# Kernel optimization log

Measured on AMD Instinct MI355X. Metric: run time of the kernel, lower is better.

## Reference

```python
import jax, jax.numpy as jnp
import numpy as np

D_MODEL = 1024
N_HEADS = 16
K_RETRIEVED = 32
BANK_SIZE = 131072
EPS = 1e-12  # matches F.normalize eps


def setup_inputs() -> dict:
    key = jax.random.key(0)
    ks = jax.random.split(key, 7)
    B, T = 8, 2048
    x = jax.random.normal(ks[0], (B, T, D_MODEL), dtype=jnp.float32)
    mem_keys = jax.random.normal(ks[1], (BANK_SIZE, D_MODEL), dtype=jnp.float32)
    mem_values = jax.random.normal(ks[2], (BANK_SIZE, D_MODEL), dtype=jnp.float32)
    s = 1.0 / np.sqrt(D_MODEL)
    Wq = jax.random.normal(ks[3], (D_MODEL, D_MODEL), dtype=jnp.float32) * s
    Wk = jax.random.normal(ks[4], (D_MODEL, D_MODEL), dtype=jnp.float32) * s
    Wv = jax.random.normal(ks[5], (D_MODEL, D_MODEL), dtype=jnp.float32) * s
    Wo = jax.random.normal(ks[6], (D_MODEL, D_MODEL), dtype=jnp.float32) * s
    gate_logit = jnp.zeros((1,), dtype=jnp.float32)
    return {"x": x, "mem_keys": mem_keys, "mem_values": mem_values,
            "Wq": Wq, "Wk": Wk, "Wv": Wv, "Wo": Wo, "gate_logit": gate_logit}


def _normalize(v):
    n = jnp.linalg.norm(v, axis=-1, keepdims=True)
    return v / jnp.maximum(n, EPS)


def reference(x, mem_keys, mem_values, Wq, Wk, Wv, Wo, gate_logit):
    B, T, D = x.shape
    H, hd, k = N_HEADS, D_MODEL // N_HEADS, K_RETRIEVED

    # --- retrieval: mean-pool query, cosine-sim top-k, gather values ---
    q = x.mean(axis=1)                       # (B, D)
    sims = _normalize(q) @ _normalize(mem_keys).T   # (B, BANK_SIZE)
    _, idx = jax.lax.top_k(sims, k)          # (B, k) descending
    retrieved = mem_values[idx]              # (B, k, d_mem)

    # --- cross-attention over retrieved docs ---
    Q = (x @ Wq).reshape(B, T, H, hd)
    K = (retrieved @ Wk).reshape(B, k, H, hd)
    V = (retrieved @ Wv).reshape(B, k, H, hd)
    scale = 1.0 / jnp.sqrt(jnp.asarray(hd, dtype=x.dtype))
    attn = jnp.einsum('bthd,bkhd->bhtk', Q, K) * scale
    attn = jax.nn.softmax(attn, axis=-1)
    ctx = jnp.einsum('bhtk,bkhd->bthd', attn, V).reshape(B, T, D)
    ctx = ctx @ Wo

    gate = jax.nn.sigmoid(gate_logit)        # (1,) broadcasts
    return x + gate * ctx
```

## Files before the change

### kernel.cpp

```cpp
#include <hip/hip_runtime.h>

#define D_MODEL 1024
#define NH 16
#define HD 64
#define KRET 32
#define BANK 131072
#define BB 8
#define TT 2048
#define MTOK 16384
#define EPSN 1e-12f

typedef __attribute__((ext_vector_type(8))) short bf16x8;
typedef __attribute__((ext_vector_type(8))) unsigned short u16x8;
typedef __attribute__((ext_vector_type(4))) float f32x4;

__device__ __forceinline__ unsigned short f2bf(float f) {
  unsigned int u = __float_as_uint(f);
  u += 0x7fffu + ((u >> 16) & 1u);
  return (unsigned short)(u >> 16);
}
__device__ __forceinline__ float bf2f(unsigned short h) {
  return __uint_as_float(((unsigned int)h) << 16);
}

__device__ __forceinline__ void gload16(const void* g, void* l) {
  __builtin_amdgcn_global_load_lds(
      (const __attribute__((address_space(1))) unsigned int*)g,
      (__attribute__((address_space(3))) unsigned int*)l, 16, 0, 0);
}

__global__ __launch_bounds__(256) void k_conv_mean(const float* __restrict__ x,
                                                   unsigned short* __restrict__ xb,
                                                   float* __restrict__ part) {
  int ch = blockIdx.x, b = blockIdx.y, tid = threadIdx.x;
  const float4* xp = (const float4*)(x + ((size_t)b * TT + ch * 32) * D_MODEL);
  ushort4* xo = (ushort4*)(xb + ((size_t)b * TT + ch * 32) * D_MODEL);
  float4 acc = {0.f, 0.f, 0.f, 0.f};
#pragma unroll 4
  for (int t = 0; t < 32; t++) {
    float4 v = xp[t * 256 + tid];
    acc.x += v.x; acc.y += v.y; acc.z += v.z; acc.w += v.w;
    ushort4 o;
    o.x = f2bf(v.x); o.y = f2bf(v.y); o.z = f2bf(v.z); o.w = f2bf(v.w);
    xo[t * 256 + tid] = o;
  }
  ((float4*)part)[((size_t)b * 64 + ch) * 256 + tid] = acc;
}

__global__ __launch_bounds__(256) void k_transW(const float* W0, const float* W1,
                                                const float* W2, const float* W3,
                                                unsigned short* T0, unsigned short* T1,
                                                unsigned short* T2, unsigned short* T3) {
  const float* W; unsigned short* T;
  switch (blockIdx.z) {
    case 0: W = W0; T = T0; break;
    case 1: W = W1; T = T1; break;
    case 2: W = W2; T = T2; break;
    default: W = W3; T = T3; break;
  }
  __shared__ float tile[64][65];
  int k0 = blockIdx.y * 64, n0 = blockIdx.x * 64;
  int tid = threadIdx.x;
#pragma unroll
  for (int i = 0; i < 16; i++) {
    int idx = tid + i * 256; int r = idx >> 6, c = idx & 63;
    tile[r][c] = W[(size_t)(k0 + r) * D_MODEL + n0 + c];
  }
  __syncthreads();
#pragma unroll
  for (int i = 0; i < 16; i++) {
    int idx = tid + i * 256; int r = idx >> 6, c = idx & 63;
    T[(size_t)(n0 + r) * D_MODEL + k0 + c] = f2bf(tile[c][r]);
  }
}

__global__ __launch_bounds__(256) void k_qnorm(const float* __restrict__ part,
                                               float* __restrict__ qn) {
  int b = blockIdx.x; int tid = threadIdx.x;
  __shared__ float red[4];
  const float4* pp = (const float4*)part + (size_t)b * 64 * 256 + tid;
  float4 a = {0.f, 0.f, 0.f, 0.f};
#pragma unroll 8
  for (int p = 0; p < 64; p++) {
    float4 v = pp[(size_t)p * 256];
    a.x += v.x; a.y += v.y; a.z += v.z; a.w += v.w;
  }
  const float sc = 1.f / (float)TT;
  a.x *= sc; a.y *= sc; a.z *= sc; a.w *= sc;
  float ss = a.x * a.x + a.y * a.y + a.z * a.z + a.w * a.w;
#pragma unroll
  for (int m = 32; m >= 1; m >>= 1) ss += __shfl_xor(ss, m);
  if ((tid & 63) == 0) red[tid >> 6] = ss;
  __syncthreads();
  float tot = red[0] + red[1] + red[2] + red[3];
  float inv = 1.f / fmaxf(sqrtf(tot), EPSN);
  float4 o = {a.x * inv, a.y * inv, a.z * inv, a.w * inv};
  ((float4*)qn)[(size_t)b * 256 + tid] = o;
}

__global__ __launch_bounds__(256) void k_sims(const float* __restrict__ mk,
                                              const float* __restrict__ qn,
                                              float* __restrict__ sims) {
  int wave = threadIdx.x >> 6, lane = threadIdx.x & 63;
  int row0 = (blockIdx.x * 4 + wave) * 4;
  float4 kv[4][4];
#pragma unroll
  for (int r = 0; r < 4; r++) {
    const float4* kr = (const float4*)(mk + (size_t)(row0 + r) * D_MODEL);
#pragma unroll
    for (int i = 0; i < 4; i++) kv[r][i] = kr[lane + 64 * i];
  }
  float ss[4] = {0.f, 0.f, 0.f, 0.f};
#pragma unroll
  for (int r = 0; r < 4; r++)
#pragma unroll
    for (int i = 0; i < 4; i++)
      ss[r] += kv[r][i].x * kv[r][i].x + kv[r][i].y * kv[r][i].y +
               kv[r][i].z * kv[r][i].z + kv[r][i].w * kv[r][i].w;
  float dots[8][4];
#pragma unroll
  for (int b = 0; b < 8; b++)
#pragma unroll
    for (int r = 0; r < 4; r++) dots[b][r] = 0.f;
#pragma unroll
  for (int b = 0; b < 8; b++) {
    const float4* qb = (const float4*)(qn + (size_t)b * D_MODEL);
#pragma unroll
    for (int i = 0; i < 4; i++) {
      float4 q4 = qb[lane + 64 * i];
#pragma unroll
      for (int r = 0; r < 4; r++)
        dots[b][r] += kv[r][i].x * q4.x + kv[r][i].y * q4.y +
                      kv[r][i].z * q4.z + kv[r][i].w * q4.w;
    }
  }
#pragma unroll
  for (int m = 32; m >= 1; m >>= 1) {
#pragma unroll
    for (int r = 0; r < 4; r++) ss[r] += __shfl_xor(ss[r], m);
#pragma unroll
    for (int b = 0; b < 8; b++)
#pragma unroll
      for (int r = 0; r < 4; r++) dots[b][r] += __shfl_xor(dots[b][r], m);
  }
  if (lane == 0) {
#pragma unroll
    for (int r = 0; r < 4; r++) {
      float inv = 1.f / fmaxf(sqrtf(ss[r]), EPSN);
#pragma unroll
      for (int b = 0; b < 8; b++)
        sims[(size_t)b * BANK + row0 + r] = dots[b][r] * inv;
    }
  }
}

__global__ __launch_bounds__(256) void k_topk_local(const float* __restrict__ sims,
                                                    float* __restrict__ cval,
                                                    int* __restrict__ cidx) {
  int b = blockIdx.y, chunk = blockIdx.x;
  int tid = threadIdx.x, wave = tid >> 6, lane = tid & 63;
  const float* sb = sims + (size_t)b * BANK + chunk * 2048;
  float v[8]; int gi[8];
#pragma unroll
  for (int j = 0; j < 8; j++) {
    int loc = j * 256 + tid;
    v[j] = sb[loc];
    gi[j] = chunk * 2048 + loc;
  }
  __shared__ float wv[4]; __shared__ int wi[4];
  __shared__ int bcast;
  for (int it = 0; it < KRET; ++it) {
    float best = -1e30f; int besti = 1 << 30;
#pragma unroll
    for (int j = 0; j < 8; j++)
      if (v[j] > best || (v[j] == best && gi[j] < besti)) { best = v[j]; besti = gi[j]; }
#pragma unroll
    for (int m = 32; m >= 1; m >>= 1) {
      float ov = __shfl_xor(best, m); int oi = __shfl_xor(besti, m);
      if (ov > best || (ov == best && oi < besti)) { best = ov; besti = oi; }
    }
    if (lane == 0) { wv[wave] = best; wi[wave] = besti; }
    __syncthreads();
    if (tid == 0) {
      float fb = wv[0]; int fi = wi[0];
      for (int w = 1; w < 4; w++)
        if (wv[w] > fb || (wv[w] == fb && wi[w] < fi)) { fb = wv[w]; fi = wi[w]; }
      bcast = fi;
      cval[((size_t)b * 64 + chunk) * KRET + it] = fb;
      cidx[((size_t)b * 64 + chunk) * KRET + it] = fi;
    }
    __syncthreads();
    int w = bcast;
#pragma unroll
    for (int j = 0; j < 8; j++)
      if (gi[j] == w) v[j] = -1e30f;
  }
}

__global__ __launch_bounds__(256) void k_topk_merge(const float* __restrict__ cval,
                                                    const int* __restrict__ cidx,
                                                    int* __restrict__ idx) {
  int b = blockIdx.x;
  int tid = threadIdx.x, wave = tid >> 6, lane = tid & 63;
  const float* cv = cval + (size_t)b * 2048;
  const int* ci = cidx + (size_t)b * 2048;
  float v[8]; int gi[8];
#pragma unroll
  for (int j = 0; j < 8; j++) {
    int loc = j * 256 + tid;
    v[j] = cv[loc];
    gi[j] = ci[loc];
  }
  __shared__ float wv[4]; __shared__ int wi[4];
  __shared__ int bcast;
  for (int it = 0; it < KRET; ++it) {
    float best = -1e30f; int besti = 1 << 30;
#pragma unroll
    for (int j = 0; j < 8; j++)
      if (v[j] > best || (v[j] == best && gi[j] < besti)) { best = v[j]; besti = gi[j]; }
#pragma unroll
    for (int m = 32; m >= 1; m >>= 1) {
      float ov = __shfl_xor(best, m); int oi = __shfl_xor(besti, m);
      if (ov > best || (ov == best && oi < besti)) { best = ov; besti = oi; }
    }
    if (lane == 0) { wv[wave] = best; wi[wave] = besti; }
    __syncthreads();
    if (tid == 0) {
      float fb = wv[0]; int fi = wi[0];
      for (int w = 1; w < 4; w++)
        if (wv[w] > fb || (wv[w] == fb && wi[w] < fi)) { fb = wv[w]; fi = wi[w]; }
      bcast = fi;
      idx[b * KRET + it] = fi;
    }
    __syncthreads();
    int w = bcast;
#pragma unroll
    for (int j = 0; j < 8; j++)
      if (gi[j] == w) v[j] = -1e30f;
  }
}

__global__ __launch_bounds__(256) void k_kvgemm(const float* __restrict__ mv,
                                                const int* __restrict__ idx_g,
                                                const unsigned short* __restrict__ Bt,
                                                float* __restrict__ Kout,
                                                float* __restrict__ Vout) {
  __shared__ __align__(16) unsigned short As[128 * 32];
  __shared__ __align__(16) unsigned short Bs[128 * 32];
  __shared__ int idxs[128];
  const int tid = threadIdx.x;
  const int wave = tid >> 6, lane = tid & 63;
  const int bm = blockIdx.x * 128, bn = blockIdx.y * 128;
  const int wm = (wave >> 1) * 64, wn = (wave & 1) * 64;
  const int frow = lane & 15, kg = lane >> 4;
  const int K = 1024;

  if (tid < 128) idxs[tid] = idx_g[bm + tid];
  __syncthreads();

  f32x4 acc[4][4] = {};

  const int row0 = tid >> 2, col0 = (tid & 3) * 8;
  const int row1 = row0 + 64;
  const int g0 = tid * 8;
  const int g1 = 2048 + tid * 8;
  const unsigned short* b0 = Bt + (size_t)(bn + (g0 >> 5)) * K + (g0 & 31);
  const unsigned short* b1 = Bt + (size_t)(bn + (g1 >> 5)) * K + (g1 & 31);
  unsigned short* lB0 = &Bs[wave * 512];
  unsigned short* lB1 = &Bs[2048 + wave * 512];
  const float* src0 = mv + (size_t)idxs[row0] * D_MODEL + col0;
  const float* src1 = mv + (size_t)idxs[row1] * D_MODEL + col0;

  for (int k0 = 0; k0 < K; k0 += 32) {
    gload16(b0 + k0, lB0);
    gload16(b1 + k0, lB1);
    float4 u0 = *(const float4*)(src0 + k0);
    float4 w0 = *(const float4*)(src0 + k0 + 4);
    float4 u1 = *(const float4*)(src1 + k0);
    float4 w1 = *(const float4*)(src1 + k0 + 4);
    u16x8 p0, p1;
    p0[0] = f2bf(u0.x); p0[1] = f2bf(u0.y); p0[2] = f2bf(u0.z); p0[3] = f2bf(u0.w);
    p0[4] = f2bf(w0.x); p0[5] = f2bf(w0.y); p0[6] = f2bf(w0.z); p0[7] = f2bf(w0.w);
    p1[0] = f2bf(u1.x); p1[1] = f2bf(u1.y); p1[2] = f2bf(u1.z); p1[3] = f2bf(u1.w);
    p1[4] = f2bf(w1.x); p1[5] = f2bf(w1.y); p1[6] = f2bf(w1.z); p1[7] = f2bf(w1.w);
    *(u16x8*)&As[row0 * 32 + col0] = p0;
    *(u16x8*)&As[row1 * 32 + col0] = p1;
    __syncthreads();
    bf16x8 fa[4], fb[4];
#pragma unroll
    for (int i = 0; i < 4; i++)
      fa[i] = *(const bf16x8*)&As[(wm + i * 16 + frow) * 32 + kg * 8];
#pragma unroll
    for (int i = 0; i < 4; i++)
      fb[i] = *(const bf16x8*)&Bs[(wn + i * 16 + frow) * 32 + kg * 8];
#pragma unroll
    for (int i = 0; i < 4; i++)
#pragma unroll
      for (int j = 0; j < 4; j++)
        acc[i][j] = __builtin_amdgcn_mfma_f32_16x16x32_bf16(fa[i], fb[j], acc[i][j], 0, 0, 0);
    __syncthreads();
  }

  const int crow = (lane >> 4) * 4, ccol = lane & 15;
#pragma unroll
  for (int i = 0; i < 4; i++)
#pragma unroll
    for (int j = 0; j < 4; j++)
#pragma unroll
      for (int r = 0; r < 4; r++) {
        int gm = bm + wm + i * 16 + crow + r;
        int gn = bn + wn + j * 16 + ccol;
        int b = gm >> 5, jj = gm & 31;
        if (gn < 1024) {
          int h = gn >> 6, d = gn & 63;
          Kout[((((size_t)b * NH + h) * KRET + jj) << 6) + d] = acc[i][j][r];
        } else {
          int gn2 = gn - 1024;
          int h = gn2 >> 6, d = gn2 & 63;
          Vout[((((size_t)b * NH + h) * KRET + jj) << 6) + d] = acc[i][j][r];
        }
      }
}

template <int MODE>
__global__ __launch_bounds__(256) void k_gemm(const unsigned short* __restrict__ A,
                                              const unsigned short* __restrict__ Bt,
                                              float* __restrict__ out_f,
                                              unsigned short* __restrict__ out_b,
                                              const float* __restrict__ xres,
                                              const float* __restrict__ gatep) {
  __shared__ __align__(16) unsigned short As[128 * 32];
  __shared__ __align__(16) unsigned short Bs[128 * 32];
  const int tid = threadIdx.x;
  const int wave = tid >> 6, lane = tid & 63;
  const int bm = blockIdx.x * 128, bn = blockIdx.y * 128;
  const int wm = (wave >> 1) * 64, wn = (wave & 1) * 64;
  const int frow = lane & 15, kg = lane >> 4;
  const int K = 1024;

  f32x4 acc[4][4] = {};

  const int g0 = tid * 8;
  const int g1 = 2048 + tid * 8;
  const unsigned short* a0 = A + (size_t)(bm + (g0 >> 5)) * K + (g0 & 31);
  const unsigned short* a1 = A + (size_t)(bm + (g1 >> 5)) * K + (g1 & 31);
  const unsigned short* b0 = Bt + (size_t)(bn + (g0 >> 5)) * K + (g0 & 31);
  const unsigned short* b1 = Bt + (size_t)(bn + (g1 >> 5)) * K + (g1 & 31);
  unsigned short* lA0 = &As[wave * 512];
  unsigned short* lA1 = &As[2048 + wave * 512];
  unsigned short* lB0 = &Bs[wave * 512];
  unsigned short* lB1 = &Bs[2048 + wave * 512];

  for (int k0 = 0; k0 < K; k0 += 32) {
    gload16(a0 + k0, lA0);
    gload16(a1 + k0, lA1);
    gload16(b0 + k0, lB0);
    gload16(b1 + k0, lB1);
    __syncthreads();
    bf16x8 fa[4], fb[4];
#pragma unroll
    for (int i = 0; i < 4; i++)
      fa[i] = *(const bf16x8*)&As[(wm + i * 16 + frow) * 32 + kg * 8];
#pragma unroll
    for (int i = 0; i < 4; i++)
      fb[i] = *(const bf16x8*)&Bs[(wn + i * 16 + frow) * 32 + kg * 8];
#pragma unroll
    for (int i = 0; i < 4; i++)
#pragma unroll
      for (int j = 0; j < 4; j++)
        acc[i][j] = __builtin_amdgcn_mfma_f32_16x16x32_bf16(fa[i], fb[j], acc[i][j], 0, 0, 0);
    __syncthreads();
  }

  const int crow = (lane >> 4) * 4, ccol = lane & 15;
  if (MODE == 2) {
    float gate = 1.f / (1.f + __expf(-gatep[0]));
#pragma unroll
    for (int i = 0; i < 4; i++)
#pragma unroll
      for (int j = 0; j < 4; j++)
#pragma unroll
        for (int r = 0; r < 4; r++) {
          int gm = bm + wm + i * 16 + crow + r;
          int gn = bn + wn + j * 16 + ccol;
          size_t off = (size_t)gm * D_MODEL + gn;
          out_f[off] = xres[off] + gate * acc[i][j][r];
        }
  } else {
#pragma unroll
    for (int i = 0; i < 4; i++)
#pragma unroll
      for (int j = 0; j < 4; j++)
#pragma unroll
        for (int r = 0; r < 4; r++) {
          int gm = bm + wm + i * 16 + crow + r;
          int gn = bn + wn + j * 16 + ccol;
          int b = gm >> 11, t = gm & 2047, h = gn >> 6, d = gn & 63;
          out_b[((((size_t)b * NH + h) * TT + t) << 6) + d] = f2bf(acc[i][j][r]);
        }
  }
}

__global__ __launch_bounds__(256) void k_attn(const unsigned short* __restrict__ Qb,
                                              const float* __restrict__ Kws,
                                              const float* __restrict__ Vws,
                                              unsigned short* __restrict__ ctx) {
  __shared__ __align__(16) unsigned short Kl[32 * 72];
  __shared__ __align__(16) unsigned short Vt[64 * 40];
  __shared__ __align__(16) unsigned short Pl[4][16 * 40];
  const int bh = blockIdx.y, b = bh >> 4, h = bh & 15;
  const int tid = threadIdx.x, wave = tid >> 6, lane = tid & 63;
  const int t0b = blockIdx.x * 256;
  {
    int doc = tid >> 3, d0 = (tid & 7) * 8;
    const float4* kp = (const float4*)(Kws + ((size_t)bh * KRET + doc) * HD + d0);
    float4 k0 = kp[0], k1 = kp[1];
    u16x8 kb;
    kb[0] = f2bf(k0.x); kb[1] = f2bf(k0.y); kb[2] = f2bf(k0.z); kb[3] = f2bf(k0.w);
    kb[4] = f2bf(k1.x); kb[5] = f2bf(k1.y); kb[6] = f2bf(k1.z); kb[7] = f2bf(k1.w);
    *(u16x8*)&Kl[doc * 72 + d0] = kb;
    const float4* vp = (const float4*)(Vws + ((size_t)bh * KRET + doc) * HD + d0);
    float4 v0 = vp[0], v1 = vp[1];
    float vv[8] = {v0.x, v0.y, v0.z, v0.w, v1.x, v1.y, v1.z, v1.w};
#pragma unroll
    for (int j = 0; j < 8; j++) Vt[(d0 + j) * 40 + doc] = f2bf(vv[j]);
  }
  __syncthreads();

  const int fr = lane & 15, kg = lane >> 4;
  const bf16x8 kb00 = *(const bf16x8*)&Kl[fr * 72 + kg * 8];
  const bf16x8 kb01 = *(const bf16x8*)&Kl[fr * 72 + 32 + kg * 8];
  const bf16x8 kb10 = *(const bf16x8*)&Kl[(16 + fr) * 72 + kg * 8];
  const bf16x8 kb11 = *(const bf16x8*)&Kl[(16 + fr) * 72 + 32 + kg * 8];
  bf16x8 vbf[4];
#pragma unroll
  for (int dt = 0; dt < 4; dt++)
    vbf[dt] = *(const bf16x8*)&Vt[(dt * 16 + fr) * 40 + kg * 8];
  unsigned short* pw = &Pl[wave][0];

#pragma unroll
  for (int sub = 0; sub < 4; ++sub) {
    const int t0 = t0b + wave * 64 + sub * 16;
    const unsigned short* qrow = Qb + ((size_t)bh * TT + t0 + fr) * HD + kg * 8;
    bf16x8 qa0 = *(const bf16x8*)(qrow);
    bf16x8 qa1 = *(const bf16x8*)(qrow + 32);
    f32x4 s0 = {}, s1 = {};
    s0 = __builtin_amdgcn_mfma_f32_16x16x32_bf16(qa0, kb00, s0, 0, 0, 0);
    s0 = __builtin_amdgcn_mfma_f32_16x16x32_bf16(qa1, kb01, s0, 0, 0, 0);
    s1 = __builtin_amdgcn_mfma_f32_16x16x32_bf16(qa0, kb10, s1, 0, 0, 0);
    s1 = __builtin_amdgcn_mfma_f32_16x16x32_bf16(qa1, kb11, s1, 0, 0, 0);
    float a0[4], a1[4], mr[4], e0[4], e1[4], sr[4];
#pragma unroll
    for (int r = 0; r < 4; r++) {
      a0[r] = s0[r] * 0.125f; a1[r] = s1[r] * 0.125f;
      mr[r] = fmaxf(a0[r], a1[r]);
    }
#pragma unroll
    for (int m = 1; m < 16; m <<= 1)
#pragma unroll
      for (int r = 0; r < 4; r++) mr[r] = fmaxf(mr[r], __shfl_xor(mr[r], m));
#pragma unroll
    for (int r = 0; r < 4; r++) {
      e0[r] = __expf(a0[r] - mr[r]); e1[r] = __expf(a1[r] - mr[r]);
      sr[r] = e0[r] + e1[r];
    }
#pragma unroll
    for (int m = 1; m < 16; m <<= 1)
#pragma unroll
      for (int r = 0; r < 4; r++) sr[r] += __shfl_xor(sr[r], m);
#pragma unroll
    for (int r = 0; r < 4; r++) {
      float inv = 1.f / sr[r];
      int tl = (lane >> 4) * 4 + r;
      pw[tl * 40 + fr] = f2bf(e0[r] * inv);
      pw[tl * 40 + 16 + fr] = f2bf(e1[r] * inv);
    }
    asm volatile("s_waitcnt lgkmcnt(0)" ::: "memory");
    bf16x8 pa = *(const bf16x8*)&pw[fr * 40 + kg * 8];
    f32x4 c[4];
#pragma unroll
    for (int dt = 0; dt < 4; dt++) {
      f32x4 z = {};
      c[dt] = __builtin_amdgcn_mfma_f32_16x16x32_bf16(pa, vbf[dt], z, 0, 0, 0);
    }
#pragma unroll
    for (int r = 0; r < 4; r++) {
      int tl = (lane >> 4) * 4 + r;
      unsigned short* crow = ctx + ((size_t)(b * TT + t0 + tl)) * D_MODEL + h * HD;
#pragma unroll
      for (int dt = 0; dt < 4; dt++)
        crow[dt * 16 + fr] = f2bf(c[dt][r]);
    }
  }
}

extern "C" void kernel_launch(void* const* d_in, const int* in_sizes, int n_in,
                              void* d_out, int out_size, void* d_ws, size_t ws_size,
                              hipStream_t stream) {
  const float* x = (const float*)d_in[0];
  const float* mk = (const float*)d_in[1];
  const float* mv = (const float*)d_in[2];
  const float* Wq = (const float*)d_in[3];
  const float* Wk = (const float*)d_in[4];
  const float* Wv = (const float*)d_in[5];
  const float* Wo = (const float*)d_in[6];
  const float* gatep = (const float*)d_in[7];
  float* out = (float*)d_out;

  char* ws = (char*)d_ws;
  unsigned short* xb   = (unsigned short*)(ws);
  unsigned short* Qb   = (unsigned short*)(ws + 33554432);
  unsigned short* WqT  = (unsigned short*)(ws + 67108864);
  unsigned short* WkvT = (unsigned short*)(ws + 69206016);
  unsigned short* WoT  = (unsigned short*)(ws + 73400320);
  float* qn    = (float*)(ws + 75497472);
  float* sims  = (float*)(ws + 75530240);
  float* part  = (float*)(ws + 75530240);
  int*   idx   = (int*)(ws + 79724544);
  float* cval  = (float*)(ws + 79725568);
  int*   cidxb = (int*)(ws + 79791104);
  float* Kws   = (float*)(ws + 79856640);
  float* Vws   = (float*)(ws + 80905216);

  k_conv_mean<<<dim3(64, 8), 256, 0, stream>>>(x, xb, part);
  k_transW<<<dim3(16, 16, 4), 256, 0, stream>>>(Wq, Wk, Wv, Wo,
                                                WqT, WkvT, WkvT + 1048576, WoT);
  k_qnorm<<<dim3(8), 256, 0, stream>>>(part, qn);
  k_sims<<<dim3(BANK / 16), 256, 0, stream>>>(mk, qn, sims);
  k_topk_local<<<dim3(64, 8), 256, 0, stream>>>(sims, cval, cidxb);
  k_topk_merge<<<dim3(8), 256, 0, stream>>>(cval, cidxb, idx);
  k_kvgemm<<<dim3(2, 16), 256, 0, stream>>>(mv, idx, WkvT, Kws, Vws);
  k_gemm<0><<<dim3(128, 8), 256, 0, stream>>>(xb, WqT, nullptr, Qb, nullptr, nullptr);
  k_attn<<<dim3(8, 128), 256, 0, stream>>>(Qb, Kws, Vws, xb);
  k_gemm<2><<<dim3(128, 8), 256, 0, stream>>>(xb, WoT, out, nullptr, x, gatep);
}
```

Measured before the change: 466.4 us.

## Replace bf16 GEMM with 256x256-tile, 8-wave, 4-stage pipelined swizzled kernel

Result: faster. 423.6 us (-9.2%).

```diff
diff --git a/kernel.cpp b/kernel.cpp
--- a/kernel.cpp
+++ b/kernel.cpp
@@ -322,81 +322,114 @@
       }
 }
 
+#define STG_A(SB, T)                                          \
+  do {                                                        \
+    const int st_ = (T) < 31 ? (T) : 31;                      \
+    gload16(aS0 + st_ * 32, &ldsA[SB][ldst0]);                \
+    gload16(aS1 + st_ * 32, &ldsA[SB][ldst1]);                \
+  } while (0)
+#define STG_B(SB, T)                                          \
+  do {                                                        \
+    const int st_ = (T) < 31 ? (T) : 31;                      \
+    gload16(bS0 + st_ * 32, &ldsB[SB][ldst0]);                \
+    gload16(bS1 + st_ * 32, &ldsB[SB][ldst1]);                \
+  } while (0)
+#define GPH(CB, I0, NEWB, STMT, VM)                                            \
+  do {                                                                         \
+    bf16x8 af[4];                                                              \
+    _Pragma("unroll") for (int ii = 0; ii < 4; ii++)                           \
+        af[ii] = *(const bf16x8*)&ldsA[CB][((wr * 128 + (I0 + ii) * 16 + fr) << 5) + (sA << 3)]; \
+    if (NEWB) {                                                                \
+      _Pragma("unroll") for (int jj = 0; jj < 4; jj++)                         \
+          bf[jj] = *(const bf16x8*)&ldsB[CB][((wc * 64 + jj * 16 + fr) << 5) + (sA << 3)]; \
+    }                                                                          \
+    STMT;                                                                      \
+    __builtin_amdgcn_s_barrier();                                              \
+    __builtin_amdgcn_s_setprio(1);                                             \
+    _Pragma("unroll") for (int ii = 0; ii < 4; ii++)                           \
+        _Pragma("unroll") for (int jj = 0; jj < 4; jj++)                       \
+            acc[I0 + ii][jj] = __builtin_amdgcn_mfma_f32_16x16x32_bf16(        \
+                af[ii], bf[jj], acc[I0 + ii][jj], 0, 0, 0);                    \
+    __builtin_amdgcn_s_setprio(0);                                             \
+    if (VM) asm volatile("s_waitcnt vmcnt(4)" ::: "memory");                   \
+    __builtin_amdgcn_s_barrier();                                              \
+  } while (0)
+
 template <int MODE>
-__global__ __launch_bounds__(256) void k_gemm(const unsigned short* __restrict__ A,
-                                              const unsigned short* __restrict__ Bt,
-                                              float* __restrict__ out_f,
-                                              unsigned short* __restrict__ out_b,
-                                              const float* __restrict__ xres,
-                                              const float* __restrict__ gatep) {
-  __shared__ __align__(16) unsigned short As[128 * 32];
-  __shared__ __align__(16) unsigned short Bs[128 * 32];
+__global__ __launch_bounds__(512, 2) void k_gemm8(const unsigned short* __restrict__ A,
+                                                  const unsigned short* __restrict__ Bt,
+                                                  float* __restrict__ out_f,
+                                                  unsigned short* __restrict__ out_b,
+                                                  const float* __restrict__ xres,
+                                                  const float* __restrict__ gatep) {
+  __shared__ __align__(16) unsigned short ldsA[4][8192];
+  __shared__ __align__(16) unsigned short ldsB[4][8192];
   const int tid = threadIdx.x;
-  const int wave = tid >> 6, lane = tid & 63;
-  const int bm = blockIdx.x * 128, bn = blockIdx.y * 128;
-  const int wm = (wave >> 1) * 64, wn = (wave & 1) * 64;
-  const int frow = lane & 15, kg = lane >> 4;
+  const int wid = tid >> 6, lane = tid & 63;
+  const int wr = wid >> 2, wc = wid & 3;
+  const int fr = lane & 15, kg = lane >> 4;
+  const int bm = blockIdx.x * 256, bn = blockIdx.y * 256;
   const int K = 1024;
 
-  f32x4 acc[4][4] = {};
-
-  const int g0 = tid * 8;
-  const int g1 = 2048 + tid * 8;
-  const unsigned short* a0 = A + (size_t)(bm + (g0 >> 5)) * K + (g0 & 31);
-  const unsigned short* a1 = A + (size_t)(bm + (g1 >> 5)) * K + (g1 & 31);
-  const unsigned short* b0 = Bt + (size_t)(bn + (g0 >> 5)) * K + (g0 & 31);
-  const unsigned short* b1 = Bt + (size_t)(bn + (g1 >> 5)) * K + (g1 & 31);
-  unsigned short* lA0 = &As[wave * 512];
-  unsigned short* lA1 = &As[2048 + wave * 512];
-  unsigned short* lB0 = &Bs[wave * 512];
-  unsigned short* lB1 = &Bs[2048 + wave * 512];
-
-  for (int k0 = 0; k0 < K; k0 += 32) {
-    gload16(a0 + k0, lA0);
-    gload16(a1 + k0, lA1);
-    gload16(b0 + k0, lB0);
-    gload16(b1 + k0, lB1);
-    __syncthreads();
-    bf16x8 fa[4], fb[4];
-#pragma unroll
-    for (int i = 0; i < 4; i++)
-      fa[i] = *(const bf16x8*)&As[(wm + i * 16 + frow) * 32 + kg * 8];
-#pragma unroll
-    for (int i = 0; i < 4; i++)
-      fb[i] = *(const bf16x8*)&Bs[(wn + i * 16 + frow) * 32 + kg * 8];
-#pragma unroll
-    for (int i = 0; i < 4; i++)
-#pragma unroll
-      for (int j = 0; j < 4; j++)
-        acc[i][j] = __builtin_amdgcn_mfma_f32_16x16x32_bf16(fa[i], fb[j], acc[i][j], 0, 0, 0);
-    __syncthreads();
+  f32x4 acc[8][4] = {};
+  bf16x8 bf[4];
+
+  const int r0 = tid >> 2, s0 = tid & 3;
+  const int sw0 = s0 ^ ((r0 >> 1) & 3);
+  const int r1 = r0 + 128;
+  const int sw1 = s0 ^ ((r1 >> 1) & 3);
+  const unsigned short* aS0 = A + (size_t)(bm + r0) * K + sw0 * 8;
+  const unsigned short* aS1 = A + (size_t)(bm + r1) * K + sw1 * 8;
+  const unsigned short* bS0 = Bt + (size_t)(bn + r0) * K + sw0 * 8;
+  const unsigned short* bS1 = Bt + (size_t)(bn + r1) * K + sw1 * 8;
+  const int ldst0 = wid << 9;
+  const int ldst1 = 4096 + (wid << 9);
+  const int sA = kg ^ ((fr >> 1) & 3);
+
+  STG_A(0, 0); STG_B(0, 0);
+  STG_A(1, 1); STG_B(1, 1);
+  STG_A(2, 2); STG_B(2, 2);
+  asm volatile("s_waitcnt vmcnt(4)" ::: "memory");
+  __builtin_amdgcn_s_barrier();
+
+#pragma unroll 1
+  for (int it = 0; it < 8; ++it) {
+    const int t = it * 4;
+    GPH(0, 0, 1, STG_A(3, t + 3), 0);
+    GPH(0, 4, 0, STG_B(3, t + 3), 0);
+    GPH(1, 0, 1, STG_A(0, t + 4), 0);
+    GPH(1, 4, 0, STG_B(0, t + 4), 1);
+    GPH(2, 0, 1, STG_A(1, t + 5), 0);
+    GPH(2, 4, 0, STG_B(1, t + 5), 0);
+    GPH(3, 0, 1, STG_A(2, t + 6), 0);
+    GPH(3, 4, 0, STG_B(2, t + 6), 1);
   }
 
   const int crow = (lane >> 4) * 4, ccol = lane & 15;
   if (MODE == 2) {
     float gate = 1.f / (1.f + __expf(-gatep[0]));
 #pragma unroll
-    for (int i = 0; i < 4; i++)
+    for (int i = 0; i < 8; i++)
 #pragma unroll
       for (int j = 0; j < 4; j++)
 #pragma unroll
         for (int r = 0; r < 4; r++) {
-          int gm = bm + wm + i * 16 + crow + r;
-          int gn = bn + wn + j * 16 + ccol;
+          int gm = bm + wr * 128 + i * 16 + crow + r;
+          int gn = bn + wc * 64 + j * 16 + ccol;
           size_t off = (size_t)gm * D_MODEL + gn;
           out_f[off] = xres[off] + gate * acc[i][j][r];
         }
   } else {
 #pragma unroll
-    for (int i = 0; i < 4; i++)
+    for (int i = 0; i < 8; i++)
 #pragma unroll
       for (int j = 0; j < 4; j++)
 #pragma unroll
         for (int r = 0; r < 4; r++) {
-          int gm = bm + wm + i * 16 + crow + r;
-          int gn = bn + wn + j * 16 + ccol;
-          int b = gm >> 11, t = gm & 2047, h = gn >> 6, d = gn & 63;
-          out_b[((((size_t)b * NH + h) * TT + t) << 6) + d] = f2bf(acc[i][j][r]);
+          int gm = bm + wr * 128 + i * 16 + crow + r;
+          int gn = bn + wc * 64 + j * 16 + ccol;
+          int b = gm >> 11, tt = gm & 2047, h = gn >> 6, d = gn & 63;
+          out_b[((((size_t)b * NH + h) * TT + tt) << 6) + d] = f2bf(acc[i][j][r]);
         }
   }
 }
@@ -530,7 +563,7 @@
   k_topk_local<<<dim3(64, 8), 256, 0, stream>>>(sims, cval, cidxb);
   k_topk_merge<<<dim3(8), 256, 0, stream>>>(cval, cidxb, idx);
   k_kvgemm<<<dim3(2, 16), 256, 0, stream>>>(mv, idx, WkvT, Kws, Vws);
-  k_gemm<0><<<dim3(128, 8), 256, 0, stream>>>(xb, WqT, nullptr, Qb, nullptr, nullptr);
+  k_gemm8<0><<<dim3(64, 4), 512, 0, stream>>>(xb, WqT, nullptr, Qb, nullptr, nullptr);
   k_attn<<<dim3(8, 128), 256, 0, stream>>>(Qb, Kws, Vws, xb);
-  k_gemm<2><<<dim3(128, 8), 256, 0, stream>>>(xb, WoT, out, nullptr, x, gatep);
-}
+  k_gemm8<2><<<dim3(64, 4), 512, 0, stream>>>(xb, WoT, out, nullptr, x, gatep);
+}
```
